# Kernel tuning notes

Hardware: AMD Instinct MI355X
Metric: run time of the kernel (lower is better)

## Reference

```python
import jax, jax.numpy as jnp
import numpy as np

B, A, D = 256, 32, 2048  # batch, num attributes, hidden_dim


def setup_inputs() -> dict:
    key = jax.random.key(0)
    k1, k2, k3, k4, k5 = jax.random.split(key, 5)
    x = jax.random.normal(k1, (B, D), dtype=jnp.float32)
    attribute_feat = jax.random.normal(k2, (B, A, D), dtype=jnp.float32)
    attribute_label = jax.random.randint(k3, (B, A), 0, 2, dtype=jnp.int64)
    # GraphConvolution parameters (glorot-style scale)
    W = jax.random.normal(k4, (D, D), dtype=jnp.float32) * (1.0 / np.sqrt(D))
    b = jnp.zeros((D,), dtype=jnp.float32)
    return {"x": x, "attribute_feat": attribute_feat,
            "attribute_label": attribute_label, "W": W, "b": b}


def reference(x, attribute_feat, attribute_label, W, b):
    # Star adjacency: nonzero attribute nodes <-> global node (index A)
    mask = (attribute_label > 0).astype(x.dtype)            # [B, A]
    adj = jnp.zeros((B, A + 1, A + 1), dtype=x.dtype)
    adj = adj.at[:, :A, A].set(mask).at[:, A, :A].set(mask)  # [B, A+1, A+1]
    # Vertex features: attributes + global node (x) per sample
    vertex = jnp.concatenate([attribute_feat, x[:, None, :]], axis=1)  # [B, A+1, D]
    # GCN layer: tanh(adj @ (vertex @ W) + b); dropout is identity in eval
    support = jnp.einsum('bnd,de->bne', vertex, W)           # [B, A+1, D]
    out = jnp.tanh(jnp.einsum('bnm,bmd->bnd', adj, support) + b)
    # Return updated global-node embedding per sample
    return out[:, -1, :]                                     # [B, D]
```

## Files before the change

kernel.cpp:

```cpp
#include <hip/hip_runtime.h>
#include <hip/hip_bf16.h>

typedef unsigned short ushort_t;
using ushort4v = __attribute__((ext_vector_type(4))) ushort_t;
using ushort8 = __attribute__((ext_vector_type(8))) ushort_t;
using short8  = __attribute__((ext_vector_type(8))) short;
using float4v = __attribute__((ext_vector_type(4))) float;

#define Bsz 256
#define Aattr 32
#define Ddim 2048
#define OUTN (Bsz * Ddim)

__device__ __forceinline__ float bf2f(ushort_t u) {
    union { unsigned int i; float f; } c;
    c.i = ((unsigned int)u) << 16;
    return c.f;
}

__device__ __forceinline__ ushort_t f2bf(float f) {
    union { float f; unsigned int i; } c;
    c.f = f;
    unsigned int x = c.i;
    unsigned int r = (x + 0x7FFFu + ((x >> 16) & 1u)) >> 16;
    return (ushort_t)r;
}

struct BfPair { ushort_t hi, lo; };
__device__ __forceinline__ BfPair split_bf16(float x) {
    BfPair p;
    p.hi = f2bf(x);
    p.lo = f2bf(x - bf2f(p.hi));
    return p;
}

__global__ __launch_bounds__(256) void k_reduce(
    const float* __restrict__ feat, const int* __restrict__ label,
    ushort_t* __restrict__ s_hi, ushort_t* __restrict__ s_lo) {
    __shared__ int list[Aattr];
    __shared__ int cnt;
    const int b = blockIdx.x;
    const int t = threadIdx.x;

    if (t < 64) {
        int lab = label[b * Aattr + (t & 31)];
        unsigned long long vote = __ballot(lab > 0);
        unsigned m32 = (unsigned)(vote & 0xFFFFFFFFull);
        if (t < 32) {
            if (lab > 0) {
                int rank = __popc(m32 & ((1u << t) - 1u));
                list[rank] = t;
            }
            if (t == 0) cnt = __popc(m32);
        }
    }
    __syncthreads();

    const int n  = cnt;
    const int d0 = blockIdx.y * 1024 + t * 4;
    const float* fb = feat + (size_t)b * (Aattr * Ddim) + d0;

    float a0 = 0.f, a1 = 0.f, a2 = 0.f, a3 = 0.f;
    int i = 0;
    for (; i + 4 <= n; i += 4) {
        const int j0 = list[i], j1 = list[i + 1], j2 = list[i + 2], j3 = list[i + 3];
        float4 v0 = *(const float4*)(fb + j0 * Ddim);
        float4 v1 = *(const float4*)(fb + j1 * Ddim);
        float4 v2 = *(const float4*)(fb + j2 * Ddim);
        float4 v3 = *(const float4*)(fb + j3 * Ddim);
        a0 += v0.x + v1.x + v2.x + v3.x;
        a1 += v0.y + v1.y + v2.y + v3.y;
        a2 += v0.z + v1.z + v2.z + v3.z;
        a3 += v0.w + v1.w + v2.w + v3.w;
    }
    for (; i < n; ++i) {
        float4 v = *(const float4*)(fb + list[i] * Ddim);
        a0 += v.x; a1 += v.y; a2 += v.z; a3 += v.w;
    }

    ushort4v hi, lo;
    BfPair p0 = split_bf16(a0); hi[0] = p0.hi; lo[0] = p0.lo;
    BfPair p1 = split_bf16(a1); hi[1] = p1.hi; lo[1] = p1.lo;
    BfPair p2 = split_bf16(a2); hi[2] = p2.hi; lo[2] = p2.lo;
    BfPair p3 = split_bf16(a3); hi[3] = p3.hi; lo[3] = p3.lo;
    *(ushort4v*)(s_hi + (size_t)b * Ddim + d0) = hi;
    *(ushort4v*)(s_lo + (size_t)b * Ddim + d0) = lo;
}

__global__ __launch_bounds__(256) void k_wt(
    const float* __restrict__ W, ushort_t* __restrict__ WT_hi,
    ushort_t* __restrict__ WT_lo) {
    __shared__ float tile[64][65];
    const int bx = blockIdx.x;
    const int by = blockIdx.y;
    const int t  = threadIdx.x;

#pragma unroll
    for (int p = 0; p < 4; ++p) {
        const int row = p * 16 + (t >> 4);
        const int c   = (t & 15) * 4;
        float4 v = *(const float4*)(W + (size_t)(by * 64 + row) * Ddim + bx * 64 + c);
        tile[row][c + 0] = v.x;
        tile[row][c + 1] = v.y;
        tile[row][c + 2] = v.z;
        tile[row][c + 3] = v.w;
    }
    __syncthreads();
#pragma unroll
    for (int p = 0; p < 2; ++p) {
        const int er = p * 32 + (t >> 3);
        const int dc = (t & 7) * 8;
        ushort8 hi, lo;
#pragma unroll
        for (int j = 0; j < 8; ++j) {
            BfPair pr = split_bf16(tile[dc + j][er]);
            hi[j] = pr.hi; lo[j] = pr.lo;
        }
        const size_t off = (size_t)(bx * 64 + er) * Ddim + by * 64 + dc;
        *(ushort8*)(WT_hi + off) = hi;
        *(ushort8*)(WT_lo + off) = lo;
    }
}

__global__ __launch_bounds__(64) void k_gemm(
    const ushort_t* __restrict__ S_hi, const ushort_t* __restrict__ S_lo,
    const ushort_t* __restrict__ WT_hi, const ushort_t* __restrict__ WT_lo,
    float* __restrict__ partials, int KS, int lks, int kchunk) {
    const int g    = blockIdx.x;
    const int ks   = g & (KS - 1);
    const int r    = g >> lks;
    const int m0   = (r & 7) * 32;
    const int n0   = (r >> 3) * 64;
    const int k0   = ks * kchunk;

    const int l    = threadIdx.x;
    const int quad = l >> 4;
    const int m16  = l & 15;

    float4v acc[2][4];
#pragma unroll
    for (int i = 0; i < 2; ++i)
#pragma unroll
        for (int j = 0; j < 4; ++j) acc[i][j] = {0.f, 0.f, 0.f, 0.f};

    const size_t aoff = (size_t)(m0 + m16) * Ddim + quad * 8;
    const size_t boff = (size_t)(n0 + m16) * Ddim + quad * 8;
    const ushort_t* Ah = S_hi + aoff;
    const ushort_t* Al = S_lo + aoff;
    const ushort_t* Bh = WT_hi + boff;
    const ushort_t* Bl = WT_lo + boff;

#pragma unroll 2
    for (int k = k0; k < k0 + kchunk; k += 32) {
        short8 ah0 = *(const short8*)(Ah + k);
        short8 ah1 = *(const short8*)(Ah + 16 * Ddim + k);
        short8 al0 = *(const short8*)(Al + k);
        short8 al1 = *(const short8*)(Al + 16 * Ddim + k);
        short8 bh0 = *(const short8*)(Bh + k);
        short8 bh1 = *(const short8*)(Bh + 16 * Ddim + k);
        short8 bh2 = *(const short8*)(Bh + 32 * Ddim + k);
        short8 bh3 = *(const short8*)(Bh + 48 * Ddim + k);
        short8 bl0 = *(const short8*)(Bl + k);
        short8 bl1 = *(const short8*)(Bl + 16 * Ddim + k);
        short8 bl2 = *(const short8*)(Bl + 32 * Ddim + k);
        short8 bl3 = *(const short8*)(Bl + 48 * Ddim + k);

        acc[0][0] = __builtin_amdgcn_mfma_f32_16x16x32_bf16(ah0, bh0, acc[0][0], 0, 0, 0);
        acc[0][1] = __builtin_amdgcn_mfma_f32_16x16x32_bf16(ah0, bh1, acc[0][1], 0, 0, 0);
        acc[0][2] = __builtin_amdgcn_mfma_f32_16x16x32_bf16(ah0, bh2, acc[0][2], 0, 0, 0);
        acc[0][3] = __builtin_amdgcn_mfma_f32_16x16x32_bf16(ah0, bh3, acc[0][3], 0, 0, 0);
        acc[1][0] = __builtin_amdgcn_mfma_f32_16x16x32_bf16(ah1, bh0, acc[1][0], 0, 0, 0);
        acc[1][1] = __builtin_amdgcn_mfma_f32_16x16x32_bf16(ah1, bh1, acc[1][1], 0, 0, 0);
        acc[1][2] = __builtin_amdgcn_mfma_f32_16x16x32_bf16(ah1, bh2, acc[1][2], 0, 0, 0);
        acc[1][3] = __builtin_amdgcn_mfma_f32_16x16x32_bf16(ah1, bh3, acc[1][3], 0, 0, 0);

        acc[0][0] = __builtin_amdgcn_mfma_f32_16x16x32_bf16(ah0, bl0, acc[0][0], 0, 0, 0);
        acc[0][1] = __builtin_amdgcn_mfma_f32_16x16x32_bf16(ah0, bl1, acc[0][1], 0, 0, 0);
        acc[0][2] = __builtin_amdgcn_mfma_f32_16x16x32_bf16(ah0, bl2, acc[0][2], 0, 0, 0);
        acc[0][3] = __builtin_amdgcn_mfma_f32_16x16x32_bf16(ah0, bl3, acc[0][3], 0, 0, 0);
        acc[1][0] = __builtin_amdgcn_mfma_f32_16x16x32_bf16(ah1, bl0, acc[1][0], 0, 0, 0);
        acc[1][1] = __builtin_amdgcn_mfma_f32_16x16x32_bf16(ah1, bl1, acc[1][1], 0, 0, 0);
        acc[1][2] = __builtin_amdgcn_mfma_f32_16x16x32_bf16(ah1, bl2, acc[1][2], 0, 0, 0);
        acc[1][3] = __builtin_amdgcn_mfma_f32_16x16x32_bf16(ah1, bl3, acc[1][3], 0, 0, 0);

        acc[0][0] = __builtin_amdgcn_mfma_f32_16x16x32_bf16(al0, bh0, acc[0][0], 0, 0, 0);
        acc[0][1] = __builtin_amdgcn_mfma_f32_16x16x32_bf16(al0, bh1, acc[0][1], 0, 0, 0);
        acc[0][2] = __builtin_amdgcn_mfma_f32_16x16x32_bf16(al0, bh2, acc[0][2], 0, 0, 0);
        acc[0][3] = __builtin_amdgcn_mfma_f32_16x16x32_bf16(al0, bh3, acc[0][3], 0, 0, 0);
        acc[1][0] = __builtin_amdgcn_mfma_f32_16x16x32_bf16(al1, bh0, acc[1][0], 0, 0, 0);
        acc[1][1] = __builtin_amdgcn_mfma_f32_16x16x32_bf16(al1, bh1, acc[1][1], 0, 0, 0);
        acc[1][2] = __builtin_amdgcn_mfma_f32_16x16x32_bf16(al1, bh2, acc[1][2], 0, 0, 0);
        acc[1][3] = __builtin_amdgcn_mfma_f32_16x16x32_bf16(al1, bh3, acc[1][3], 0, 0, 0);
    }

    float* pout = partials + (size_t)ks * OUTN;
#pragma unroll
    for (int mi = 0; mi < 2; ++mi) {
#pragma unroll
        for (int ni = 0; ni < 4; ++ni) {
            const int n = n0 + ni * 16 + m16;
#pragma unroll
            for (int rr = 0; rr < 4; ++rr) {
                const int m = m0 + mi * 16 + quad * 4 + rr;
                pout[(size_t)m * Ddim + n] = acc[mi][ni][rr];
            }
        }
    }
}

__global__ __launch_bounds__(256) void k_finish(
    const float* __restrict__ partials, const float* __restrict__ bias,
    float* __restrict__ out, int KS) {
    const int i = (blockIdx.x * 256 + threadIdx.x) * 4;
    float a0 = 0.f, a1 = 0.f, a2 = 0.f, a3 = 0.f;
    for (int s = 0; s < KS; ++s) {
        float4 v = *(const float4*)(partials + (size_t)s * OUTN + i);
        a0 += v.x; a1 += v.y; a2 += v.z; a3 += v.w;
    }
    float4 bv = *(const float4*)(bias + (i & (Ddim - 1)));
    float4 o;
    o.x = tanhf(a0 + bv.x);
    o.y = tanhf(a1 + bv.y);
    o.z = tanhf(a2 + bv.z);
    o.w = tanhf(a3 + bv.w);
    *(float4*)(out + i) = o;
}

extern "C" void kernel_launch(void* const* d_in, const int* in_sizes, int n_in,
                              void* d_out, int out_size, void* d_ws, size_t ws_size,
                              hipStream_t stream) {
    const float* feat  = (const float*)d_in[1];
    const int*   label = (const int*)d_in[2];
    const float* W     = (const float*)d_in[3];
    const float* bias  = (const float*)d_in[4];
    float*       out   = (float*)d_out;

    char* ws = (char*)d_ws;
    ushort_t* s_hi  = (ushort_t*)ws;
    ushort_t* s_lo  = (ushort_t*)(ws + (1u << 20));
    ushort_t* WT_hi = (ushort_t*)(ws + (2u << 20));
    ushort_t* WT_lo = (ushort_t*)(ws + (10u << 20));
    float* partials = (float*)(ws + (18u << 20));

    const size_t avail = ws_size > (18u << 20) ? ws_size - (18u << 20) : 0;
    int KS = 1, lks = 0;
    while (KS < 8 && (size_t)(KS * 2) * (OUTN * sizeof(float)) <= avail) { KS *= 2; ++lks; }
    const int kchunk = Ddim / KS;

    k_reduce<<<dim3(Bsz, 2), dim3(256), 0, stream>>>(feat, label, s_hi, s_lo);
    k_wt<<<dim3(32, 32), dim3(256), 0, stream>>>(W, WT_hi, WT_lo);
    k_gemm<<<dim3(256 * KS), dim3(64), 0, stream>>>(s_hi, s_lo, WT_hi, WT_lo,
                                                    partials, KS, lks, kchunk);
    k_finish<<<dim3(OUTN / 1024), dim3(256), 0, stream>>>(partials, bias, out, KS);
}
```

Baseline: 144.4 us.

## Merge reduce and W-transpose kernels; enlarge GEMM wave tile to 64x64

Folds the masked attribute reduction and the W transpose/bf16 split into one launch by dispatching on block index, which removes one kernel launch and lets the two independent prep stages run concurrently. The GEMM tile per wave grows from 32x64 to 64x64 with 16 accumulators, so each loaded A/B fragment is reused across more MFMAs, and the grid is halved. The larger tile raises register pressure, cuts the number of waves in flight (128*KS single-wave blocks), and drops the explicit unroll, which may reduce latency hiding.

Result: faster. 138.8 us (-3.9%).

```diff
diff --git a/kernel.cpp b/kernel.cpp
--- a/kernel.cpp
+++ b/kernel.cpp
@@ -34,91 +34,93 @@
     return p;
 }
 
-__global__ __launch_bounds__(256) void k_reduce(
+__global__ __launch_bounds__(256) void k_prep(
     const float* __restrict__ feat, const int* __restrict__ label,
-    ushort_t* __restrict__ s_hi, ushort_t* __restrict__ s_lo) {
-    __shared__ int list[Aattr];
-    __shared__ int cnt;
-    const int b = blockIdx.x;
+    const float* __restrict__ W,
+    ushort_t* __restrict__ s_hi, ushort_t* __restrict__ s_lo,
+    ushort_t* __restrict__ WT_hi, ushort_t* __restrict__ WT_lo) {
+    __shared__ float tile[64][65];
     const int t = threadIdx.x;
 
-    if (t < 64) {
-        int lab = label[b * Aattr + (t & 31)];
-        unsigned long long vote = __ballot(lab > 0);
-        unsigned m32 = (unsigned)(vote & 0xFFFFFFFFull);
-        if (t < 32) {
-            if (lab > 0) {
-                int rank = __popc(m32 & ((1u << t) - 1u));
-                list[rank] = t;
-            }
-            if (t == 0) cnt = __popc(m32);
-        }
-    }
-    __syncthreads();
-
-    const int n  = cnt;
-    const int d0 = blockIdx.y * 1024 + t * 4;
-    const float* fb = feat + (size_t)b * (Aattr * Ddim) + d0;
-
-    float a0 = 0.f, a1 = 0.f, a2 = 0.f, a3 = 0.f;
-    int i = 0;
-    for (; i + 4 <= n; i += 4) {
-        const int j0 = list[i], j1 = list[i + 1], j2 = list[i + 2], j3 = list[i + 3];
-        float4 v0 = *(const float4*)(fb + j0 * Ddim);
-        float4 v1 = *(const float4*)(fb + j1 * Ddim);
-        float4 v2 = *(const float4*)(fb + j2 * Ddim);
-        float4 v3 = *(const float4*)(fb + j3 * Ddim);
-        a0 += v0.x + v1.x + v2.x + v3.x;
-        a1 += v0.y + v1.y + v2.y + v3.y;
-        a2 += v0.z + v1.z + v2.z + v3.z;
-        a3 += v0.w + v1.w + v2.w + v3.w;
-    }
-    for (; i < n; ++i) {
-        float4 v = *(const float4*)(fb + list[i] * Ddim);
-        a0 += v.x; a1 += v.y; a2 += v.z; a3 += v.w;
-    }
-
-    ushort4v hi, lo;
-    BfPair p0 = split_bf16(a0); hi[0] = p0.hi; lo[0] = p0.lo;
-    BfPair p1 = split_bf16(a1); hi[1] = p1.hi; lo[1] = p1.lo;
-    BfPair p2 = split_bf16(a2); hi[2] = p2.hi; lo[2] = p2.lo;
-    BfPair p3 = split_bf16(a3); hi[3] = p3.hi; lo[3] = p3.lo;
-    *(ushort4v*)(s_hi + (size_t)b * Ddim + d0) = hi;
-    *(ushort4v*)(s_lo + (size_t)b * Ddim + d0) = lo;
-}
-
-__global__ __launch_bounds__(256) void k_wt(
-    const float* __restrict__ W, ushort_t* __restrict__ WT_hi,
-    ushort_t* __restrict__ WT_lo) {
-    __shared__ float tile[64][65];
-    const int bx = blockIdx.x;
-    const int by = blockIdx.y;
-    const int t  = threadIdx.x;
-
-#pragma unroll
-    for (int p = 0; p < 4; ++p) {
-        const int row = p * 16 + (t >> 4);
-        const int c   = (t & 15) * 4;
-        float4 v = *(const float4*)(W + (size_t)(by * 64 + row) * Ddim + bx * 64 + c);
-        tile[row][c + 0] = v.x;
-        tile[row][c + 1] = v.y;
-        tile[row][c + 2] = v.z;
-        tile[row][c + 3] = v.w;
-    }
-    __syncthreads();
-#pragma unroll
-    for (int p = 0; p < 2; ++p) {
-        const int er = p * 32 + (t >> 3);
-        const int dc = (t & 7) * 8;
-        ushort8 hi, lo;
-#pragma unroll
-        for (int j = 0; j < 8; ++j) {
-            BfPair pr = split_bf16(tile[dc + j][er]);
-            hi[j] = pr.hi; lo[j] = pr.lo;
-        }
-        const size_t off = (size_t)(bx * 64 + er) * Ddim + by * 64 + dc;
-        *(ushort8*)(WT_hi + off) = hi;
-        *(ushort8*)(WT_lo + off) = lo;
+    if (blockIdx.x < 512) {
+        int* list = (int*)&tile[0][0];
+        int* cntp = (int*)&tile[1][0];
+        const int b    = blockIdx.x >> 1;
+        const int half = blockIdx.x & 1;
+
+        if (t < 64) {
+            int lab = label[b * Aattr + (t & 31)];
+            unsigned long long vote = __ballot(lab > 0);
+            unsigned m32 = (unsigned)(vote & 0xFFFFFFFFull);
+            if (t < 32) {
+                if (lab > 0) {
+                    int rank = __popc(m32 & ((1u << t) - 1u));
+                    list[rank] = t;
+                }
+                if (t == 0) *cntp = __popc(m32);
+            }
+        }
+        __syncthreads();
+
+        const int n  = *cntp;
+        const int d0 = half * 1024 + t * 4;
+        const float* fb = feat + (size_t)b * (Aattr * Ddim) + d0;
+
+        float a0 = 0.f, a1 = 0.f, a2 = 0.f, a3 = 0.f;
+        int i = 0;
+        for (; i + 4 <= n; i += 4) {
+            const int j0 = list[i], j1 = list[i+1], j2 = list[i+2], j3 = list[i+3];
+            float4 v0 = *(const float4*)(fb + j0 * Ddim);
+            float4 v1 = *(const float4*)(fb + j1 * Ddim);
+            float4 v2 = *(const float4*)(fb + j2 * Ddim);
+            float4 v3 = *(const float4*)(fb + j3 * Ddim);
+            a0 += v0.x + v1.x + v2.x + v3.x;
+            a1 += v0.y + v1.y + v2.y + v3.y;
+            a2 += v0.z + v1.z + v2.z + v3.z;
+            a3 += v0.w + v1.w + v2.w + v3.w;
+        }
+        for (; i < n; ++i) {
+            float4 v = *(const float4*)(fb + list[i] * Ddim);
+            a0 += v.x; a1 += v.y; a2 += v.z; a3 += v.w;
+        }
+
+        ushort4v hi, lo;
+        BfPair p0 = split_bf16(a0); hi[0] = p0.hi; lo[0] = p0.lo;
+        BfPair p1 = split_bf16(a1); hi[1] = p1.hi; lo[1] = p1.lo;
+        BfPair p2 = split_bf16(a2); hi[2] = p2.hi; lo[2] = p2.lo;
+        BfPair p3 = split_bf16(a3); hi[3] = p3.hi; lo[3] = p3.lo;
+        *(ushort4v*)(s_hi + (size_t)b * Ddim + d0) = hi;
+        *(ushort4v*)(s_lo + (size_t)b * Ddim + d0) = lo;
+    } else {
+        const int q  = blockIdx.x - 512;
+        const int bx = q & 31;
+        const int by = q >> 5;
+
+#pragma unroll
+        for (int p = 0; p < 4; ++p) {
+            const int row = p * 16 + (t >> 4);
+            const int c   = (t & 15) * 4;
+            float4 v = *(const float4*)(W + (size_t)(by * 64 + row) * Ddim + bx * 64 + c);
+            tile[row][c + 0] = v.x;
+            tile[row][c + 1] = v.y;
+            tile[row][c + 2] = v.z;
+            tile[row][c + 3] = v.w;
+        }
+        __syncthreads();
+#pragma unroll
+        for (int p = 0; p < 2; ++p) {
+            const int er = p * 32 + (t >> 3);
+            const int dc = (t & 7) * 8;
+            ushort8 hi, lo;
+#pragma unroll
+            for (int j = 0; j < 8; ++j) {
+                BfPair pr = split_bf16(tile[dc + j][er]);
+                hi[j] = pr.hi; lo[j] = pr.lo;
+            }
+            const size_t off = (size_t)(bx * 64 + er) * Ddim + by * 64 + dc;
+            *(ushort8*)(WT_hi + off) = hi;
+            *(ushort8*)(WT_lo + off) = lo;
+        }
     }
 }
 
@@ -129,17 +131,17 @@
     const int g    = blockIdx.x;
     const int ks   = g & (KS - 1);
     const int r    = g >> lks;
-    const int m0   = (r & 7) * 32;
-    const int n0   = (r >> 3) * 64;
+    const int m0   = (r & 3) * 64;
+    const int n0   = (r >> 2) * 64;
     const int k0   = ks * kchunk;
 
     const int l    = threadIdx.x;
     const int quad = l >> 4;
     const int m16  = l & 15;
 
-    float4v acc[2][4];
-#pragma unroll
-    for (int i = 0; i < 2; ++i)
+    float4v acc[4][4];
+#pragma unroll
+    for (int i = 0; i < 4; ++i)
 #pragma unroll
         for (int j = 0; j < 4; ++j) acc[i][j] = {0.f, 0.f, 0.f, 0.f};
 
@@ -150,52 +152,30 @@
     const ushort_t* Bh = WT_hi + boff;
     const ushort_t* Bl = WT_lo + boff;
 
-#pragma unroll 2
     for (int k = k0; k < k0 + kchunk; k += 32) {
-        short8 ah0 = *(const short8*)(Ah + k);
-        short8 ah1 = *(const short8*)(Ah + 16 * Ddim + k);
-        short8 al0 = *(const short8*)(Al + k);
-        short8 al1 = *(const short8*)(Al + 16 * Ddim + k);
-        short8 bh0 = *(const short8*)(Bh + k);
-        short8 bh1 = *(const short8*)(Bh + 16 * Ddim + k);
-        short8 bh2 = *(const short8*)(Bh + 32 * Ddim + k);
-        short8 bh3 = *(const short8*)(Bh + 48 * Ddim + k);
-        short8 bl0 = *(const short8*)(Bl + k);
-        short8 bl1 = *(const short8*)(Bl + 16 * Ddim + k);
-        short8 bl2 = *(const short8*)(Bl + 32 * Ddim + k);
-        short8 bl3 = *(const short8*)(Bl + 48 * Ddim + k);
-
-        acc[0][0] = __builtin_amdgcn_mfma_f32_16x16x32_bf16(ah0, bh0, acc[0][0], 0, 0, 0);
-        acc[0][1] = __builtin_amdgcn_mfma_f32_16x16x32_bf16(ah0, bh1, acc[0][1], 0, 0, 0);
-        acc[0][2] = __builtin_amdgcn_mfma_f32_16x16x32_bf16(ah0, bh2, acc[0][2], 0, 0, 0);
-        acc[0][3] = __builtin_amdgcn_mfma_f32_16x16x32_bf16(ah0, bh3, acc[0][3], 0, 0, 0);
-        acc[1][0] = __builtin_amdgcn_mfma_f32_16x16x32_bf16(ah1, bh0, acc[1][0], 0, 0, 0);
-        acc[1][1] = __builtin_amdgcn_mfma_f32_16x16x32_bf16(ah1, bh1, acc[1][1], 0, 0, 0);
-        acc[1][2] = __builtin_amdgcn_mfma_f32_16x16x32_bf16(ah1, bh2, acc[1][2], 0, 0, 0);
-        acc[1][3] = __builtin_amdgcn_mfma_f32_16x16x32_bf16(ah1, bh3, acc[1][3], 0, 0, 0);
-
-        acc[0][0] = __builtin_amdgcn_mfma_f32_16x16x32_bf16(ah0, bl0, acc[0][0], 0, 0, 0);
-        acc[0][1] = __builtin_amdgcn_mfma_f32_16x16x32_bf16(ah0, bl1, acc[0][1], 0, 0, 0);
-        acc[0][2] = __builtin_amdgcn_mfma_f32_16x16x32_bf16(ah0, bl2, acc[0][2], 0, 0, 0);
-        acc[0][3] = __builtin_amdgcn_mfma_f32_16x16x32_bf16(ah0, bl3, acc[0][3], 0, 0, 0);
-        acc[1][0] = __builtin_amdgcn_mfma_f32_16x16x32_bf16(ah1, bl0, acc[1][0], 0, 0, 0);
-        acc[1][1] = __builtin_amdgcn_mfma_f32_16x16x32_bf16(ah1, bl1, acc[1][1], 0, 0, 0);
-        acc[1][2] = __builtin_amdgcn_mfma_f32_16x16x32_bf16(ah1, bl2, acc[1][2], 0, 0, 0);
-        acc[1][3] = __builtin_amdgcn_mfma_f32_16x16x32_bf16(ah1, bl3, acc[1][3], 0, 0, 0);
-
-        acc[0][0] = __builtin_amdgcn_mfma_f32_16x16x32_bf16(al0, bh0, acc[0][0], 0, 0, 0);
-        acc[0][1] = __builtin_amdgcn_mfma_f32_16x16x32_bf16(al0, bh1, acc[0][1], 0, 0, 0);
-        acc[0][2] = __builtin_amdgcn_mfma_f32_16x16x32_bf16(al0, bh2, acc[0][2], 0, 0, 0);
-        acc[0][3] = __builtin_amdgcn_mfma_f32_16x16x32_bf16(al0, bh3, acc[0][3], 0, 0, 0);
-        acc[1][0] = __builtin_amdgcn_mfma_f32_16x16x32_bf16(al1, bh0, acc[1][0], 0, 0, 0);
-        acc[1][1] = __builtin_amdgcn_mfma_f32_16x16x32_bf16(al1, bh1, acc[1][1], 0, 0, 0);
-        acc[1][2] = __builtin_amdgcn_mfma_f32_16x16x32_bf16(al1, bh2, acc[1][2], 0, 0, 0);
-        acc[1][3] = __builtin_amdgcn_mfma_f32_16x16x32_bf16(al1, bh3, acc[1][3], 0, 0, 0);
+        short8 ah[4], al[4], bh[4], bl[4];
+#pragma unroll
+        for (int i = 0; i < 4; ++i) {
+            const size_t o = (size_t)(i * 16) * Ddim + k;
+            ah[i] = *(const short8*)(Ah + o);
+            al[i] = *(const short8*)(Al + o);
+            bh[i] = *(const short8*)(Bh + o);
+            bl[i] = *(const short8*)(Bl + o);
+        }
+#pragma unroll
+        for (int mi = 0; mi < 4; ++mi) {
+#pragma unroll
+            for (int ni = 0; ni < 4; ++ni) {
+                acc[mi][ni] = __builtin_amdgcn_mfma_f32_16x16x32_bf16(ah[mi], bh[ni], acc[mi][ni], 0, 0, 0);
+                acc[mi][ni] = __builtin_amdgcn_mfma_f32_16x16x32_bf16(ah[mi], bl[ni], acc[mi][ni], 0, 0, 0);
+                acc[mi][ni] = __builtin_amdgcn_mfma_f32_16x16x32_bf16(al[mi], bh[ni], acc[mi][ni], 0, 0, 0);
+            }
+        }
     }
 
     float* pout = partials + (size_t)ks * OUTN;
 #pragma unroll
-    for (int mi = 0; mi < 2; ++mi) {
+    for (int mi = 0; mi < 4; ++mi) {
 #pragma unroll
         for (int ni = 0; ni < 4; ++ni) {
             const int n = n0 + ni * 16 + m16;
@@ -247,9 +227,8 @@
     while (KS < 8 && (size_t)(KS * 2) * (OUTN * sizeof(float)) <= avail) { KS *= 2; ++lks; }
     const int kchunk = Ddim / KS;
 
-    k_reduce<<<dim3(Bsz, 2), dim3(256), 0, stream>>>(feat, label, s_hi, s_lo);
-    k_wt<<<dim3(32, 32), dim3(256), 0, stream>>>(W, WT_hi, WT_lo);
-    k_gemm<<<dim3(256 * KS), dim3(64), 0, stream>>>(s_hi, s_lo, WT_hi, WT_lo,
+    k_prep<<<dim3(1536), dim3(256), 0, stream>>>(feat, label, W, s_hi, s_lo, WT_hi, WT_lo);
+    k_gemm<<<dim3(128 * KS), dim3(64), 0, stream>>>(s_hi, s_lo, WT_hi, WT_lo,
                                                     partials, KS, lks, kchunk);
     k_finish<<<dim3(OUTN / 1024), dim3(256), 0, stream>>>(partials, bias, out, KS);
 }
```
